# Performance work log

Hardware: AMD Instinct MI355X
Metric: run time of the kernel (lower is better)

## Reference

```python
import jax, jax.numpy as jnp
import numpy as np

B, N_CAPS, N_VOTES, D_IN, D_H, D_CP = 1024, 64, 36, 256, 128, 32
TWO_PI = 2.0 * np.pi


def geometric_transform(pose):
    # pose: [..., 6] -> affine 3x3 matrix [..., 3, 3] (nonlinear, full affine)
    sx, sy, theta, shear, tx, ty = jnp.split(pose, 6, axis=-1)
    sx = jax.nn.sigmoid(sx) + 1e-2
    sy = jax.nn.sigmoid(sy) + 1e-2
    tx = jnp.tanh(tx * 5.0)
    ty = jnp.tanh(ty * 5.0)
    shear = jnp.tanh(shear * 5.0)
    theta = theta * TWO_PI
    c, s = jnp.cos(theta), jnp.sin(theta)
    row0 = jnp.concatenate([sx * c + shear * sy * s, -sx * s + shear * sy * c, tx], -1)
    row1 = jnp.concatenate([sy * s, sy * c, ty], -1)
    zeros = jnp.zeros_like(tx)
    row2 = jnp.concatenate([zeros, zeros, jnp.ones_like(tx)], -1)
    return jnp.stack([row0, row1, row2], axis=-2)


def setup_inputs() -> dict:
    key = jax.random.key(0)
    ks = jax.random.split(key, 16)
    u = lambda k, shp: 0.5 * (jax.random.uniform(k, shp, jnp.float32) - 0.5)
    return {
        "features": jax.random.normal(ks[0], (B, N_CAPS, D_IN), jnp.float32),
        "w1": u(ks[1], (1, N_CAPS, D_IN, D_H)),
        "b1": jnp.zeros((1, N_CAPS, 1, D_H), jnp.float32),
        "w2": u(ks[2], (1, N_CAPS, D_H, D_CP)),
        "b2": jnp.zeros((1, N_CAPS, 1, D_CP), jnp.float32),
        "caps_mlp_w": u(ks[3], (1, N_CAPS, D_CP + 1, D_H)),
        "caps_mlp_b": jnp.zeros((1, N_CAPS, 1, D_H), jnp.float32),
        "cpr_dynamic_w": u(ks[4], (1, N_CAPS, D_H, N_VOTES * 6)),
        "ccr_w": u(ks[5], (1, N_CAPS, D_H, 6)),
        "ccr_b": jnp.zeros((1, N_CAPS, 1, 6), jnp.float32),
        "pres_caps_w": u(ks[6], (1, N_CAPS, D_H, 1)),
        "pres_caps_b": jnp.zeros((1, N_CAPS, 1, 1), jnp.float32),
        "pres_vote_w": u(ks[7], (1, N_CAPS, D_H, N_VOTES)),
        "pres_vote_b": jnp.zeros((1, N_CAPS, 1, N_VOTES), jnp.float32),
        "scale_vote_w": u(ks[8], (1, N_CAPS, D_H, N_VOTES)),
        "scale_vote_b": jnp.zeros((1, N_CAPS, 1, N_VOTES), jnp.float32),
        "cpr_static": jax.random.uniform(ks[9], (1, N_CAPS, N_VOTES, 6), jnp.float32) - 0.5,
    }


def reference(features, w1, b1, w2, b2, caps_mlp_w, caps_mlp_b, cpr_dynamic_w,
              ccr_w, ccr_b, pres_caps_w, pres_caps_b, pres_vote_w, pres_vote_b,
              scale_vote_w, scale_vote_b, cpr_static):
    batch_size = features.shape[0]
    x = features[:, :, None, :]                               # [B, C, 1, 256]
    h = jax.nn.relu(x @ w1 + b1)                              # [B, C, 1, H]
    raw_caps_params = jax.nn.relu(h @ w2 + b2)                # [B, C, 1, P]
    caps_exist = jnp.ones(raw_caps_params.shape[:-1] + (1,), raw_caps_params.dtype)
    caps_params = jnp.concatenate([raw_caps_params, caps_exist], -1)  # [B, C, 1, P+1]
    caps_feat = jax.nn.relu(caps_params @ caps_mlp_w + caps_mlp_b)    # [B, C, 1, H]

    cpr_dynamic = (caps_feat @ cpr_dynamic_w).reshape(batch_size, N_CAPS, N_VOTES, 6)
    ccr = caps_feat @ ccr_w + ccr_b                           # [B, C, 1, 6]
    pres_logit_per_caps = (caps_feat @ pres_caps_w + pres_caps_b)[:, :, 0, :]   # [B, C, 1]
    pres_logit_per_vote = (caps_feat @ pres_vote_w + pres_vote_b)[:, :, 0, :]   # [B, C, V]
    scale_per_vote = (caps_feat @ scale_vote_w + scale_vote_b)[:, :, 0, :]      # [B, C, V]

    ccr_mat = geometric_transform(ccr)                        # [B, C, 1, 3, 3]
    cpr_mat = geometric_transform(cpr_dynamic + cpr_static)   # [B, C, V, 3, 3]
    votes = ccr_mat @ cpr_mat                                 # [B, C, V, 3, 3]

    pres_per_caps = jax.nn.sigmoid(pres_logit_per_caps)
    pres_per_vote = pres_per_caps * jax.nn.sigmoid(pres_logit_per_vote)
    scale_per_vote = jax.nn.softplus(scale_per_vote + 0.5) + 0.01
    dynamic_weights_l2 = jnp.sum(cpr_dynamic ** 2) / batch_size / 2.0
    return (votes, scale_per_vote, pres_per_vote, pres_logit_per_caps,
            pres_logit_per_vote, dynamic_weights_l2, raw_caps_params[:, :, 0, :], features)
```

## Files before the change

kernel.cpp:

```cpp
#include <hip/hip_runtime.h>
#include <math.h>

#define NB   1024
#define NC   64
#define DIN  256
#define DH   128
#define DCP  32
#define NV   36

#define OFF0 0
#define OFF1 21233664
#define OFF2 23592960
#define OFF3 25952256
#define OFF4 26017792
#define OFF5 28377088
#define OFF6 28377089
#define OFF7 30474241

#define SM_FST  0
#define SM_M    4224
#define SM_PSIG 4416
#define SM_CPS  4448
#define SM_XS   5536
#define SM_W1C  6592
#define SM_W2S  5536
#define SM_WM   5536
#define SM_WH   5536
#define SM_HD   8096
#define SM_HB   10656
#define SM_WD   5536
#define SM_DYN  8992
#define SM_TOT  15904

__device__ __forceinline__ float sigm(float x) { return 1.0f / (1.0f + __expf(-x)); }
__device__ __forceinline__ float tanh5(float x) {
    x = fminf(fmaxf(5.0f * x, -15.0f), 15.0f);
    float z = __expf(2.0f * x);
    return (z - 1.0f) / (z + 1.0f);
}
__device__ __forceinline__ void geo(const float* p, float* m) {
    float sx = sigm(p[0]) + 0.01f;
    float sy = sigm(p[1]) + 0.01f;
    float th = p[2] * 6.28318530717958647692f;
    float sh = tanh5(p[3]);
    float tx = tanh5(p[4]);
    float ty = tanh5(p[5]);
    float cc = __cosf(th), ss = __sinf(th);
    m[0] =  sx * cc + sh * sy * ss;
    m[1] = -sx * ss + sh * sy * cc;
    m[2] = tx;
    m[3] = sy * ss;
    m[4] = sy * cc;
    m[5] = ty;
}

__global__ void zero_l2_kernel(float* out) { out[OFF5] = 0.0f; }

__global__ __launch_bounds__(256)
void caps_fused_kernel(const float* __restrict__ feat,
                       const float* __restrict__ w1,  const float* __restrict__ b1,
                       const float* __restrict__ w2,  const float* __restrict__ b2,
                       const float* __restrict__ wm,  const float* __restrict__ bm,
                       const float* __restrict__ wdy,
                       const float* __restrict__ wccr,const float* __restrict__ bccr,
                       const float* __restrict__ wpc, const float* __restrict__ bpc,
                       const float* __restrict__ wpv, const float* __restrict__ bpv,
                       const float* __restrict__ wsv, const float* __restrict__ bsv,
                       const float* __restrict__ cst,
                       float* __restrict__ out)
{
    __shared__ float sm[SM_TOT];
    const int t  = threadIdx.x;
    const int c  = blockIdx.y;
    const int rb = blockIdx.x * 32;

    {
        const int tx = t & 31;
        const int ty = t >> 5;
        float acc[4][4] = {};
        const int xrow = t >> 3, xk4 = (t & 7) << 2;
        for (int k0 = 0; k0 < DIN; k0 += 32) {
            __syncthreads();
            {
                const int gi = (rb + xrow) * (NC * DIN) + c * DIN + k0 + xk4;
                const float4 v = *(const float4*)&feat[gi];
                float* xs = &sm[SM_XS + xrow * 33 + xk4];
                xs[0] = v.x; xs[1] = v.y; xs[2] = v.z; xs[3] = v.w;
                float* o7 = &out[OFF7 + gi];
                o7[0] = v.x; o7[1] = v.y; o7[2] = v.z; o7[3] = v.w;
            }
#pragma unroll
            for (int p = 0; p < 4; ++p) {
                const int idx = t + p * 256;
                *(float4*)&sm[SM_W1C + idx * 4] =
                    *(const float4*)&w1[c * (DIN * DH) + k0 * DH + idx * 4];
            }
            __syncthreads();
#pragma unroll 8
            for (int kk = 0; kk < 32; ++kk) {
                const float a0 = sm[SM_XS + (ty * 4 + 0) * 33 + kk];
                const float a1 = sm[SM_XS + (ty * 4 + 1) * 33 + kk];
                const float a2 = sm[SM_XS + (ty * 4 + 2) * 33 + kk];
                const float a3 = sm[SM_XS + (ty * 4 + 3) * 33 + kk];
                const float4 bv = *(const float4*)&sm[SM_W1C + kk * DH + tx * 4];
                acc[0][0] += a0 * bv.x; acc[0][1] += a0 * bv.y; acc[0][2] += a0 * bv.z; acc[0][3] += a0 * bv.w;
                acc[1][0] += a1 * bv.x; acc[1][1] += a1 * bv.y; acc[1][2] += a1 * bv.z; acc[1][3] += a1 * bv.w;
                acc[2][0] += a2 * bv.x; acc[2][1] += a2 * bv.y; acc[2][2] += a2 * bv.z; acc[2][3] += a2 * bv.w;
                acc[3][0] += a3 * bv.x; acc[3][1] += a3 * bv.y; acc[3][2] += a3 * bv.z; acc[3][3] += a3 * bv.w;
            }
        }
        const float4 bb4 = *(const float4*)&b1[c * DH + tx * 4];
        const float bb[4] = { bb4.x, bb4.y, bb4.z, bb4.w };
#pragma unroll
        for (int i = 0; i < 4; ++i)
#pragma unroll
            for (int j = 0; j < 4; ++j) {
                float v = fmaxf(acc[i][j] + bb[j], 0.0f);
                sm[SM_FST + (tx * 4 + j) * 33 + (ty * 4 + i)] = v;
            }
    }
    __syncthreads();

#pragma unroll
    for (int p = 0; p < 4; ++p) {
        const int idx = t + p * 256;
        *(float4*)&sm[SM_W2S + idx * 4] = *(const float4*)&w2[c * (DH * DCP) + idx * 4];
    }
    __syncthreads();
    {
        const int b = t & 31;
        const int j4 = (t >> 5) << 2;
        float acc[4] = {};
#pragma unroll 8
        for (int k = 0; k < DH; ++k) {
            const float h = sm[SM_FST + k * 33 + b];
            const float4 wv = *(const float4*)&sm[SM_W2S + k * DCP + j4];
            acc[0] += h * wv.x; acc[1] += h * wv.y; acc[2] += h * wv.z; acc[3] += h * wv.w;
        }
#pragma unroll
        for (int jj = 0; jj < 4; ++jj) {
            const float v = fmaxf(acc[jj] + b2[c * DCP + j4 + jj], 0.0f);
            out[OFF6 + ((rb + b) * NC + c) * DCP + j4 + jj] = v;
            sm[SM_CPS + b * 34 + j4 + jj] = v;
        }
        if (t < 32) sm[SM_CPS + t * 34 + 32] = 1.0f;
    }
    __syncthreads();

#pragma unroll
    for (int p = 0; p < 5; ++p) {
        const int idx = t + p * 256;
        if (idx < 1056)
            *(float4*)&sm[SM_WM + idx * 4] = *(const float4*)&wm[c * (33 * DH) + idx * 4];
    }
    __syncthreads();
    {
        const int b = t & 31;
        const int nb = (t >> 5) << 4;
        float acc[16] = {};
        for (int k = 0; k < 33; ++k) {
            const float a = sm[SM_CPS + b * 34 + k];
#pragma unroll
            for (int jq = 0; jq < 4; ++jq) {
                const float4 wv = *(const float4*)&sm[SM_WM + k * DH + nb + jq * 4];
                acc[jq*4+0] += a * wv.x; acc[jq*4+1] += a * wv.y;
                acc[jq*4+2] += a * wv.z; acc[jq*4+3] += a * wv.w;
            }
        }
#pragma unroll
        for (int j = 0; j < 16; ++j) {
            const float v = fmaxf(acc[j] + bm[c * DH + nb + j], 0.0f);
            sm[SM_FST + (nb + j) * 33 + b] = v;
        }
    }
    __syncthreads();

    if (t < 80) {
        float v = 0.0f;
        if (t < 6)       v = bccr[c * 6 + t];
        else if (t == 6) v = bpc[c];
        else if (t < 43) v = bpv[c * NV + (t - 7)];
        else if (t < 79) v = bsv[c * NV + (t - 43)];
        sm[SM_HB + t] = v;
    }
    {
        const int txx = t & 15;
        const int tyy = t >> 4;
        float acc[2][5] = {};
        for (int k0 = 0; k0 < DH; k0 += 32) {
            __syncthreads();
#pragma unroll
            for (int p = 0; p < 10; ++p) {
                const int idx = t + p * 256;
                const int kk = idx / 80, col = idx % 80;
                const int kg = k0 + kk;
                float v = 0.0f;
                if (col < 6)        v = wccr[c * (DH * 6) + kg * 6 + col];
                else if (col == 6)  v = wpc[c * DH + kg];
                else if (col < 43)  v = wpv[c * (DH * NV) + kg * NV + (col - 7)];
                else if (col < 79)  v = wsv[c * (DH * NV) + kg * NV + (col - 43)];
                sm[SM_WH + kk * 80 + col] = v;
            }
            __syncthreads();
#pragma unroll 4
            for (int kk = 0; kk < 32; ++kk) {
                const float a0 = sm[SM_FST + (k0 + kk) * 33 + tyy * 2 + 0];
                const float a1 = sm[SM_FST + (k0 + kk) * 33 + tyy * 2 + 1];
#pragma unroll
                for (int j = 0; j < 5; ++j) {
                    const float w = sm[SM_WH + kk * 80 + txx * 5 + j];
                    acc[0][j] += a0 * w;
                    acc[1][j] += a1 * w;
                }
            }
        }
#pragma unroll
        for (int i = 0; i < 2; ++i)
#pragma unroll
            for (int j = 0; j < 5; ++j)
                sm[SM_HD + (tyy * 2 + i) * 80 + txx * 5 + j] = acc[i][j];
    }
    __syncthreads();

    if (t < 32) {
        const int b = t;
        const float plc = sm[SM_HD + b * 80 + 6] + sm[SM_HB + 6];
        out[OFF3 + (rb + b) * NC + c] = plc;
        sm[SM_PSIG + b] = sigm(plc);
        float p[6], m[6];
#pragma unroll
        for (int i = 0; i < 6; ++i) p[i] = sm[SM_HD + b * 80 + i] + sm[SM_HB + i];
        geo(p, m);
#pragma unroll
        for (int i = 0; i < 6; ++i) sm[SM_M + b * 6 + i] = m[i];
    }
    __syncthreads();

#pragma unroll
    for (int p = 0; p < 10; ++p) {
        const int item = t + p * 256;
        const int b = item / 80, col = item % 80;
        if (col >= 7 && col < 79) {
            const float v = sm[SM_HD + b * 80 + col] + sm[SM_HB + col];
            const int base = ((rb + b) * NC + c) * NV;
            if (col < 43) {
                const int o = col - 7;
                out[OFF4 + base + o] = v;
                out[OFF2 + base + o] = sm[SM_PSIG + b] * sigm(v);
            } else {
                const int o = col - 43;
                float sp = v + 0.5f;
                sp = (sp > 15.0f) ? sp : log1pf(__expf(sp));
                out[OFF1 + base + o] = sp + 0.01f;
            }
        }
    }
    __syncthreads();

    float l2loc = 0.0f;
    {
        const int txx = t & 31;
        const int tyy = t >> 5;
        float acc[4][7] = {};
        for (int k0 = 0; k0 < DH; k0 += 16) {
            __syncthreads();
#pragma unroll
            for (int p = 0; p < 14; ++p) {
                const int idx = t + p * 256;
                if (idx < 3456)
                    sm[SM_WD + idx] = wdy[c * (DH * 216) + k0 * 216 + idx];
            }
            __syncthreads();
#pragma unroll 4
            for (int kk = 0; kk < 16; ++kk) {
                const float a0 = sm[SM_FST + (k0 + kk) * 33 + tyy * 4 + 0];
                const float a1 = sm[SM_FST + (k0 + kk) * 33 + tyy * 4 + 1];
                const float a2 = sm[SM_FST + (k0 + kk) * 33 + tyy * 4 + 2];
                const float a3 = sm[SM_FST + (k0 + kk) * 33 + tyy * 4 + 3];
#pragma unroll
                for (int j = 0; j < 7; ++j) {
                    const int cc = min(txx * 7 + j, 215);
                    const float w = sm[SM_WD + kk * 216 + cc];
                    acc[0][j] += a0 * w;
                    acc[1][j] += a1 * w;
                    acc[2][j] += a2 * w;
                    acc[3][j] += a3 * w;
                }
            }
        }
#pragma unroll
        for (int i = 0; i < 4; ++i)
#pragma unroll
            for (int j = 0; j < 7; ++j) {
                const int cc = txx * 7 + j;
                if (cc < 216)
                    sm[SM_DYN + (tyy * 4 + i) * 216 + cc] = acc[i][j];
            }
    }
    __syncthreads();

#pragma unroll
    for (int p = 0; p < 5; ++p) {
        const int item = t + p * 256;
        if (item < 32 * NV) {
            const int b = item / NV, v = item % NV;
            float dyn[6], pose[6], mB[6];
            float ss = 0.0f;
#pragma unroll
            for (int j = 0; j < 6; ++j) {
                dyn[j] = sm[SM_DYN + b * 216 + v * 6 + j];
                ss += dyn[j] * dyn[j];
                pose[j] = dyn[j] + cst[c * (NV * 6) + v * 6 + j];
            }
            l2loc += ss;
            geo(pose, mB);
            const float A0 = sm[SM_M + b * 6 + 0], A1 = sm[SM_M + b * 6 + 1];
            const float A2 = sm[SM_M + b * 6 + 2], A3 = sm[SM_M + b * 6 + 3];
            const float A4 = sm[SM_M + b * 6 + 4], A5 = sm[SM_M + b * 6 + 5];
            const int ob = (((rb + b) * NC + c) * NV + v) * 9;
            out[OFF0 + ob + 0] = A0 * mB[0] + A1 * mB[3];
            out[OFF0 + ob + 1] = A0 * mB[1] + A1 * mB[4];
            out[OFF0 + ob + 2] = A0 * mB[2] + A1 * mB[5] + A2;
            out[OFF0 + ob + 3] = A3 * mB[0] + A4 * mB[3];
            out[OFF0 + ob + 4] = A3 * mB[1] + A4 * mB[4];
            out[OFF0 + ob + 5] = A3 * mB[2] + A4 * mB[5] + A5;
            out[OFF0 + ob + 6] = 0.0f;
            out[OFF0 + ob + 7] = 0.0f;
            out[OFF0 + ob + 8] = 1.0f;
        }
    }

    l2loc += __shfl_down(l2loc, 32, 64);
    l2loc += __shfl_down(l2loc, 16, 64);
    l2loc += __shfl_down(l2loc, 8, 64);
    l2loc += __shfl_down(l2loc, 4, 64);
    l2loc += __shfl_down(l2loc, 2, 64);
    l2loc += __shfl_down(l2loc, 1, 64);
    if ((t & 63) == 0) atomicAdd(&out[OFF5], l2loc * (1.0f / 2048.0f));
}

extern "C" void kernel_launch(void* const* d_in, const int* in_sizes, int n_in,
                              void* d_out, int out_size, void* d_ws, size_t ws_size,
                              hipStream_t stream)
{
    const float* feat = (const float*)d_in[0];
    const float* w1   = (const float*)d_in[1];
    const float* b1   = (const float*)d_in[2];
    const float* w2   = (const float*)d_in[3];
    const float* b2   = (const float*)d_in[4];
    const float* wm   = (const float*)d_in[5];
    const float* bm   = (const float*)d_in[6];
    const float* wdy  = (const float*)d_in[7];
    const float* wccr = (const float*)d_in[8];
    const float* bccr = (const float*)d_in[9];
    const float* wpc  = (const float*)d_in[10];
    const float* bpc  = (const float*)d_in[11];
    const float* wpv  = (const float*)d_in[12];
    const float* bpv  = (const float*)d_in[13];
    const float* wsv  = (const float*)d_in[14];
    const float* bsv  = (const float*)d_in[15];
    const float* cst  = (const float*)d_in[16];
    float* out = (float*)d_out;

    zero_l2_kernel<<<1, 1, 0, stream>>>(out);
    dim3 grid(NB / 32, NC);
    caps_fused_kernel<<<grid, 256, 0, stream>>>(feat, w1, b1, w2, b2, wm, bm, wdy,
                                                wccr, bccr, wpc, bpc, wpv, bpv,
                                                wsv, bsv, cst, out);
}
```

Baseline: 656.1 us.

## Shrink shared-memory footprint via smaller K-tiles and split dynamic-pose epilogue

```diff
diff --git a/kernel.cpp b/kernel.cpp
--- a/kernel.cpp
+++ b/kernel.cpp
@@ -17,20 +17,23 @@
 #define OFF6 28377089
 #define OFF7 30474241
 
-#define SM_FST  0
-#define SM_M    4224
-#define SM_PSIG 4416
-#define SM_CPS  4448
-#define SM_XS   5536
-#define SM_W1C  6592
-#define SM_W2S  5536
-#define SM_WM   5536
-#define SM_WH   5536
-#define SM_HD   8096
-#define SM_HB   10656
-#define SM_WD   5536
-#define SM_DYN  8992
-#define SM_TOT  15904
+#define SM_FST 0
+#define SM_R2  4224
+#define SM_R3  8576
+#define SM_TOT 9664
+
+#define SM_XS  SM_R2
+#define SM_W1C (SM_R2 + 544)
+#define SM_W2S SM_R2
+#define SM_WM  SM_R2
+#define SM_WH  SM_R2
+#define SM_HD  (SM_R2 + 1280)
+#define SM_HB  (SM_R2 + 3872)
+#define SM_WD  SM_R2
+#define SM_DYN SM_R2
+#define SM_CPS SM_R3
+#define SM_M   SM_R3
+#define SM_PSIG (SM_R3 + 192)
 
 __device__ __forceinline__ float sigm(float x) { return 1.0f / (1.0f + __expf(-x)); }
 __device__ __forceinline__ float tanh5(float x) {
@@ -56,7 +59,7 @@
 
 __global__ void zero_l2_kernel(float* out) { out[OFF5] = 0.0f; }
 
-__global__ __launch_bounds__(256)
+__global__ __launch_bounds__(256, 4)
 void caps_fused_kernel(const float* __restrict__ feat,
                        const float* __restrict__ w1,  const float* __restrict__ b1,
                        const float* __restrict__ w2,  const float* __restrict__ b2,
@@ -78,30 +81,28 @@
         const int tx = t & 31;
         const int ty = t >> 5;
         float acc[4][4] = {};
-        const int xrow = t >> 3, xk4 = (t & 7) << 2;
-        for (int k0 = 0; k0 < DIN; k0 += 32) {
+        const int xrow = t >> 3, xk2 = (t & 7) * 2;
+        for (int k0 = 0; k0 < DIN; k0 += 16) {
             __syncthreads();
             {
-                const int gi = (rb + xrow) * (NC * DIN) + c * DIN + k0 + xk4;
-                const float4 v = *(const float4*)&feat[gi];
-                float* xs = &sm[SM_XS + xrow * 33 + xk4];
-                xs[0] = v.x; xs[1] = v.y; xs[2] = v.z; xs[3] = v.w;
-                float* o7 = &out[OFF7 + gi];
-                o7[0] = v.x; o7[1] = v.y; o7[2] = v.z; o7[3] = v.w;
-            }
-#pragma unroll
-            for (int p = 0; p < 4; ++p) {
-                const int idx = t + p * 256;
-                *(float4*)&sm[SM_W1C + idx * 4] =
-                    *(const float4*)&w1[c * (DIN * DH) + k0 * DH + idx * 4];
-            }
-            __syncthreads();
-#pragma unroll 8
-            for (int kk = 0; kk < 32; ++kk) {
-                const float a0 = sm[SM_XS + (ty * 4 + 0) * 33 + kk];
-                const float a1 = sm[SM_XS + (ty * 4 + 1) * 33 + kk];
-                const float a2 = sm[SM_XS + (ty * 4 + 2) * 33 + kk];
-                const float a3 = sm[SM_XS + (ty * 4 + 3) * 33 + kk];
+                const int gi = (rb + xrow) * (NC * DIN) + c * DIN + k0 + xk2;
+                const float2 v = *(const float2*)&feat[gi];
+                sm[SM_XS + xrow * 17 + xk2]     = v.x;
+                sm[SM_XS + xrow * 17 + xk2 + 1] = v.y;
+                out[OFF7 + gi]     = v.x;
+                out[OFF7 + gi + 1] = v.y;
+            }
+            *(float4*)&sm[SM_W1C + t * 4] =
+                *(const float4*)&w1[c * (DIN * DH) + k0 * DH + t * 4];
+            *(float4*)&sm[SM_W1C + (t + 256) * 4] =
+                *(const float4*)&w1[c * (DIN * DH) + k0 * DH + (t + 256) * 4];
+            __syncthreads();
+#pragma unroll
+            for (int kk = 0; kk < 16; ++kk) {
+                const float a0 = sm[SM_XS + (ty * 4 + 0) * 17 + kk];
+                const float a1 = sm[SM_XS + (ty * 4 + 1) * 17 + kk];
+                const float a2 = sm[SM_XS + (ty * 4 + 2) * 17 + kk];
+                const float a3 = sm[SM_XS + (ty * 4 + 3) * 17 + kk];
                 const float4 bv = *(const float4*)&sm[SM_W1C + kk * DH + tx * 4];
                 acc[0][0] += a0 * bv.x; acc[0][1] += a0 * bv.y; acc[0][2] += a0 * bv.z; acc[0][3] += a0 * bv.w;
                 acc[1][0] += a1 * bv.x; acc[1][1] += a1 * bv.y; acc[1][2] += a1 * bv.z; acc[1][3] += a1 * bv.w;
@@ -128,7 +129,7 @@
     }
     __syncthreads();
     {
-        const int b = t & 31;
+        const int b  = t & 31;
         const int j4 = (t >> 5) << 2;
         float acc[4] = {};
 #pragma unroll 8
@@ -155,7 +156,7 @@
     }
     __syncthreads();
     {
-        const int b = t & 31;
+        const int b  = t & 31;
         const int nb = (t >> 5) << 4;
         float acc[16] = {};
         for (int k = 0; k < 33; ++k) {
@@ -175,22 +176,14 @@
     }
     __syncthreads();
 
-    if (t < 80) {
-        float v = 0.0f;
-        if (t < 6)       v = bccr[c * 6 + t];
-        else if (t == 6) v = bpc[c];
-        else if (t < 43) v = bpv[c * NV + (t - 7)];
-        else if (t < 79) v = bsv[c * NV + (t - 43)];
-        sm[SM_HB + t] = v;
-    }
     {
         const int txx = t & 15;
         const int tyy = t >> 4;
         float acc[2][5] = {};
-        for (int k0 = 0; k0 < DH; k0 += 32) {
-            __syncthreads();
-#pragma unroll
-            for (int p = 0; p < 10; ++p) {
+        for (int k0 = 0; k0 < DH; k0 += 16) {
+            __syncthreads();
+#pragma unroll
+            for (int p = 0; p < 5; ++p) {
                 const int idx = t + p * 256;
                 const int kk = idx / 80, col = idx % 80;
                 const int kg = k0 + kk;
@@ -201,9 +194,17 @@
                 else if (col < 79)  v = wsv[c * (DH * NV) + kg * NV + (col - 43)];
                 sm[SM_WH + kk * 80 + col] = v;
             }
-            __syncthreads();
-#pragma unroll 4
-            for (int kk = 0; kk < 32; ++kk) {
+            if (k0 == 0 && t < 80) {
+                float v = 0.0f;
+                if (t < 6)       v = bccr[c * 6 + t];
+                else if (t == 6) v = bpc[c];
+                else if (t < 43) v = bpv[c * NV + (t - 7)];
+                else if (t < 79) v = bsv[c * NV + (t - 43)];
+                sm[SM_HB + t] = v;
+            }
+            __syncthreads();
+#pragma unroll
+            for (int kk = 0; kk < 16; ++kk) {
                 const float a0 = sm[SM_FST + (k0 + kk) * 33 + tyy * 2 + 0];
                 const float a1 = sm[SM_FST + (k0 + kk) * 33 + tyy * 2 + 1];
 #pragma unroll
@@ -218,18 +219,18 @@
         for (int i = 0; i < 2; ++i)
 #pragma unroll
             for (int j = 0; j < 5; ++j)
-                sm[SM_HD + (tyy * 2 + i) * 80 + txx * 5 + j] = acc[i][j];
+                sm[SM_HD + (tyy * 2 + i) * 81 + txx * 5 + j] = acc[i][j];
     }
     __syncthreads();
 
     if (t < 32) {
         const int b = t;
-        const float plc = sm[SM_HD + b * 80 + 6] + sm[SM_HB + 6];
+        const float plc = sm[SM_HD + b * 81 + 6] + sm[SM_HB + 6];
         out[OFF3 + (rb + b) * NC + c] = plc;
         sm[SM_PSIG + b] = sigm(plc);
         float p[6], m[6];
 #pragma unroll
-        for (int i = 0; i < 6; ++i) p[i] = sm[SM_HD + b * 80 + i] + sm[SM_HB + i];
+        for (int i = 0; i < 6; ++i) p[i] = sm[SM_HD + b * 81 + i] + sm[SM_HB + i];
         geo(p, m);
 #pragma unroll
         for (int i = 0; i < 6; ++i) sm[SM_M + b * 6 + i] = m[i];
@@ -241,7 +242,7 @@
         const int item = t + p * 256;
         const int b = item / 80, col = item % 80;
         if (col >= 7 && col < 79) {
-            const float v = sm[SM_HD + b * 80 + col] + sm[SM_HB + col];
+            const float v = sm[SM_HD + b * 81 + col] + sm[SM_HB + col];
             const int base = ((rb + b) * NC + c) * NV;
             if (col < 43) {
                 const int o = col - 7;
@@ -255,78 +256,80 @@
             }
         }
     }
-    __syncthreads();
 
     float l2loc = 0.0f;
     {
-        const int txx = t & 31;
-        const int tyy = t >> 5;
-        float acc[4][7] = {};
+        const int g   = t & 63;
+        const int ty4 = t >> 6;
+        float acc[8][4] = {};
         for (int k0 = 0; k0 < DH; k0 += 16) {
             __syncthreads();
 #pragma unroll
-            for (int p = 0; p < 14; ++p) {
-                const int idx = t + p * 256;
-                if (idx < 3456)
-                    sm[SM_WD + idx] = wdy[c * (DH * 216) + k0 * 216 + idx];
-            }
-            __syncthreads();
-#pragma unroll 4
+            for (int p = 0; p < 7; ++p) {
+                const int i2  = t + p * 256;
+                const int col = (i2 * 2) % 224;
+                const int row = (i2 * 2) / 224;
+                float2 v = make_float2(0.0f, 0.0f);
+                if (col < 216)
+                    v = *(const float2*)&wdy[c * (DH * 216) + (k0 + row) * 216 + col];
+                *(float2*)&sm[SM_WD + row * 224 + col] = v;
+            }
+            __syncthreads();
+#pragma unroll
             for (int kk = 0; kk < 16; ++kk) {
-                const float a0 = sm[SM_FST + (k0 + kk) * 33 + tyy * 4 + 0];
-                const float a1 = sm[SM_FST + (k0 + kk) * 33 + tyy * 4 + 1];
-                const float a2 = sm[SM_FST + (k0 + kk) * 33 + tyy * 4 + 2];
-                const float a3 = sm[SM_FST + (k0 + kk) * 33 + tyy * 4 + 3];
-#pragma unroll
-                for (int j = 0; j < 7; ++j) {
-                    const int cc = min(txx * 7 + j, 215);
-                    const float w = sm[SM_WD + kk * 216 + cc];
-                    acc[0][j] += a0 * w;
-                    acc[1][j] += a1 * w;
-                    acc[2][j] += a2 * w;
-                    acc[3][j] += a3 * w;
+                float a[8];
+#pragma unroll
+                for (int i = 0; i < 8; ++i)
+                    a[i] = sm[SM_FST + (k0 + kk) * 33 + ty4 * 8 + i];
+                const float4 w = *(const float4*)&sm[SM_WD + kk * 224 + g * 4];
+#pragma unroll
+                for (int i = 0; i < 8; ++i) {
+                    acc[i][0] += a[i] * w.x; acc[i][1] += a[i] * w.y;
+                    acc[i][2] += a[i] * w.z; acc[i][3] += a[i] * w.w;
                 }
             }
         }
-#pragma unroll
-        for (int i = 0; i < 4; ++i)
-#pragma unroll
-            for (int j = 0; j < 7; ++j) {
-                const int cc = txx * 7 + j;
-                if (cc < 216)
-                    sm[SM_DYN + (tyy * 4 + i) * 216 + cc] = acc[i][j];
-            }
-    }
-    __syncthreads();
-
-#pragma unroll
-    for (int p = 0; p < 5; ++p) {
-        const int item = t + p * 256;
-        if (item < 32 * NV) {
-            const int b = item / NV, v = item % NV;
-            float dyn[6], pose[6], mB[6];
-            float ss = 0.0f;
-#pragma unroll
-            for (int j = 0; j < 6; ++j) {
-                dyn[j] = sm[SM_DYN + b * 216 + v * 6 + j];
-                ss += dyn[j] * dyn[j];
-                pose[j] = dyn[j] + cst[c * (NV * 6) + v * 6 + j];
-            }
-            l2loc += ss;
-            geo(pose, mB);
-            const float A0 = sm[SM_M + b * 6 + 0], A1 = sm[SM_M + b * 6 + 1];
-            const float A2 = sm[SM_M + b * 6 + 2], A3 = sm[SM_M + b * 6 + 3];
-            const float A4 = sm[SM_M + b * 6 + 4], A5 = sm[SM_M + b * 6 + 5];
-            const int ob = (((rb + b) * NC + c) * NV + v) * 9;
-            out[OFF0 + ob + 0] = A0 * mB[0] + A1 * mB[3];
-            out[OFF0 + ob + 1] = A0 * mB[1] + A1 * mB[4];
-            out[OFF0 + ob + 2] = A0 * mB[2] + A1 * mB[5] + A2;
-            out[OFF0 + ob + 3] = A3 * mB[0] + A4 * mB[3];
-            out[OFF0 + ob + 4] = A3 * mB[1] + A4 * mB[4];
-            out[OFF0 + ob + 5] = A3 * mB[2] + A4 * mB[5] + A5;
-            out[OFF0 + ob + 6] = 0.0f;
-            out[OFF0 + ob + 7] = 0.0f;
-            out[OFF0 + ob + 8] = 1.0f;
+        for (int half = 0; half < 2; ++half) {
+            __syncthreads();
+            if (g < 54 && (g >= 27) == (half == 1)) {
+#pragma unroll
+                for (int i = 0; i < 8; ++i)
+#pragma unroll
+                    for (int j = 0; j < 4; ++j)
+                        sm[SM_DYN + (ty4 * 8 + i) * 109 + (g * 4 + j - half * 108)] = acc[i][j];
+            }
+            __syncthreads();
+#pragma unroll
+            for (int p = 0; p < 3; ++p) {
+                const int item = t + p * 256;
+                if (item < 576) {
+                    const int b = item / 18, vh = item % 18;
+                    const int v = half * 18 + vh;
+                    float dyn[6], pose[6], mB[6];
+                    float ss = 0.0f;
+#pragma unroll
+                    for (int j = 0; j < 6; ++j) {
+                        dyn[j] = sm[SM_DYN + b * 109 + vh * 6 + j];
+                        ss += dyn[j] * dyn[j];
+                        pose[j] = dyn[j] + cst[c * (NV * 6) + v * 6 + j];
+                    }
+                    l2loc += ss;
+                    geo(pose, mB);
+                    const float A0 = sm[SM_M + b * 6 + 0], A1 = sm[SM_M + b * 6 + 1];
+                    const float A2 = sm[SM_M + b * 6 + 2], A3 = sm[SM_M + b * 6 + 3];
+                    const float A4 = sm[SM_M + b * 6 + 4], A5 = sm[SM_M + b * 6 + 5];
+                    const int ob = (((rb + b) * NC + c) * NV + v) * 9;
+                    out[OFF0 + ob + 0] = A0 * mB[0] + A1 * mB[3];
+                    out[OFF0 + ob + 1] = A0 * mB[1] + A1 * mB[4];
+                    out[OFF0 + ob + 2] = A0 * mB[2] + A1 * mB[5] + A2;
+                    out[OFF0 + ob + 3] = A3 * mB[0] + A4 * mB[3];
+                    out[OFF0 + ob + 4] = A3 * mB[1] + A4 * mB[4];
+                    out[OFF0 + ob + 5] = A3 * mB[2] + A4 * mB[5] + A5;
+                    out[OFF0 + ob + 6] = 0.0f;
+                    out[OFF0 + ob + 7] = 0.0f;
+                    out[OFF0 + ob + 8] = 1.0f;
+                }
+            }
         }
     }
 
```

After: 622.3 us. 5.2% less time.
